# Optimization experiments

Measured on AMD Instinct MI355X. Metric: run time of the kernel, lower is better.

## Reference

```python
import jax, jax.numpy as jnp
import numpy as np

jax.config.update("jax_enable_x64", True)

PRIME = (1 << 31) - 1  # Mersenne prime; products with <2^31 operands fit in int64
N_DIGITS = 16
N_ARY = 32
EMB = 64
NUM_EMB = 100000    # importance-weight table rows
NUM_BUCKETS = 65536  # shared bucket table rows
NUM_HASHES = 2

_rng = np.random.RandomState(42)
SEQ_A = jnp.asarray(_rng.randint(1, PRIME, size=(N_DIGITS,)), dtype=jnp.int64)   # per-position keys for prefix hash
HASH_A = jnp.asarray(_rng.randint(1, PRIME, size=(NUM_HASHES,)), dtype=jnp.int64)
HASH_B = jnp.asarray(_rng.randint(0, PRIME, size=(NUM_HASHES,)), dtype=jnp.int64)


def _prefix_hashes(seq):
    # seq: [B, D] int64 sense codes, 0 = padding (mask_zero: zeros contribute nothing)
    h = jnp.cumsum(SEQ_A[None, :] * (seq.astype(jnp.int64) % PRIME), axis=-1) % PRIME  # [B, D]
    # pad_trailing_zeroes=True: positions past the code length repeat the last valid hash
    lengths = jnp.sum(seq != 0, axis=-1, keepdims=True)               # [B, 1]
    pos = jnp.arange(seq.shape[-1], dtype=jnp.int64)[None, :]
    idx = jnp.minimum(pos, jnp.maximum(lengths - 1, 0))
    return jnp.take_along_axis(h, idx, axis=-1)                        # [B, D]


def setup_inputs() -> dict:
    key = jax.random.key(0)
    k1, k2, k3, k4 = jax.random.split(key, 4)
    B = 4096
    input_sequence = jax.random.randint(k1, (B, N_DIGITS), 0, N_ARY, dtype=jnp.int64)
    t_representation = jax.random.normal(k2, (B, N_DIGITS, EMB), dtype=jnp.float32)
    importance_weights = jax.random.normal(k3, (NUM_EMB, NUM_HASHES), dtype=jnp.float32)
    bucket_table = jax.random.normal(k4, (NUM_BUCKETS, N_ARY * EMB), dtype=jnp.float32) * 0.02
    return {
        "input_sequence": input_sequence,
        "t_representation": t_representation,
        "importance_weights": importance_weights,
        "bucket_table": bucket_table,
    }


def reference(input_sequence, t_representation, importance_weights, bucket_table):
    ids = _prefix_hashes(input_sequence)                  # [B, D] prefix hash ids
    w = importance_weights[ids % NUM_EMB]                 # [B, D, H] importance weights
    emb = jnp.zeros(ids.shape + (bucket_table.shape[-1],), dtype=bucket_table.dtype)
    for h in range(NUM_HASHES):
        bucket = ((HASH_A[h] * ids + HASH_B[h]) % PRIME) % NUM_BUCKETS
        emb = emb + w[..., h:h + 1] * bucket_table[bucket]  # [B, D, N_ARY*EMB]
    B, D = ids.shape
    t_weight = emb.reshape(B, D, N_ARY, EMB).astype(t_representation.dtype)
    # torch.matmul(t_weight, rep.unsqueeze(-1)).squeeze(-1) -> [B, D, N_ARY]
    return jnp.einsum('bdae,bde->bda', t_weight, t_representation)
```

## Files before the change

### kernel.cpp

```cpp
#include <hip/hip_runtime.h>
#include <stdint.h>

#define PRIME 2147483647LL
#define NUM_EMB 100000
#define NUM_BUCKETS 65536
#define EMB 64
#define N_ARY 32
#define NDIG 16

struct HashConsts {
  long long seqA[NDIG];
  long long hashA[2];
  long long hashB[2];
};

__global__ __launch_bounds__(256) void hash_logits_kernel(
    const int* __restrict__ seq,
    const float* __restrict__ rep,
    const float* __restrict__ iw,
    const float* __restrict__ bt,
    float* __restrict__ out,
    HashConsts hc)
{
  const int bid  = blockIdx.x;
  const int b    = bid >> 2;
  const int wave = threadIdx.x >> 6;
  const int d    = ((bid & 3) << 2) | wave;
  const int lane = threadIdx.x & 63;
  const int g    = lane >> 4;
  const int sub  = lane & 15;

  const int* srow = seq + b * NDIG;
  int v[NDIG];
  int len = 0;
#pragma unroll
  for (int j = 0; j < NDIG; ++j) { v[j] = srow[j]; len += (v[j] != 0); }
  int idx = min(d, max(len - 1, 0));
  long long acc = 0;
#pragma unroll
  for (int j = 0; j < NDIG; ++j) {
    if (j <= idx) acc += hc.seqA[j] * (long long)v[j];
  }
  const long long id = acc % PRIME;

  const int widx = (int)(id % NUM_EMB);
  const float w0 = iw[widx * 2 + 0];
  const float w1 = iw[widx * 2 + 1];
  const unsigned int bk0 =
      (unsigned int)((hc.hashA[0] * id + hc.hashB[0]) % PRIME) & (NUM_BUCKETS - 1);
  const unsigned int bk1 =
      (unsigned int)((hc.hashA[1] * id + hc.hashB[1]) % PRIME) & (NUM_BUCKETS - 1);

  const float4* row0 = (const float4*)(bt + (size_t)bk0 * (N_ARY * EMB));
  const float4* row1 = (const float4*)(bt + (size_t)bk1 * (N_ARY * EMB));
  const float4 r = *(const float4*)(rep + ((size_t)b * NDIG + d) * EMB + sub * 4);

  float s[8];
#pragma unroll
  for (int k = 0; k < 8; ++k) {
    float4 v0 = row0[lane + 64 * k];
    float4 v1 = row1[lane + 64 * k];
    float ex = w0 * v0.x + w1 * v1.x;
    float ey = w0 * v0.y + w1 * v1.y;
    float ez = w0 * v0.z + w1 * v1.z;
    float ew = w0 * v0.w + w1 * v1.w;
    s[k] = ex * r.x + ey * r.y + ez * r.z + ew * r.w;
  }
#pragma unroll
  for (int m = 1; m <= 8; m <<= 1) {
#pragma unroll
    for (int k = 0; k < 8; ++k) s[k] += __shfl_xor(s[k], m, 64);
  }
  if (sub == 0) {
    float* obase = out + ((size_t)b * NDIG + d) * N_ARY + g;
#pragma unroll
    for (int k = 0; k < 8; ++k) obase[4 * k] = s[k];
  }
}

extern "C" void kernel_launch(void* const* d_in, const int* in_sizes, int n_in,
                              void* d_out, int out_size, void* d_ws, size_t ws_size,
                              hipStream_t stream) {
  uint32_t mt[624];
  int mti;
  mt[0] = 42u;
  for (int i = 1; i < 624; ++i)
    mt[i] = 1812433253u * (mt[i - 1] ^ (mt[i - 1] >> 30)) + (uint32_t)i;
  mti = 624;
  auto next32 = [&]() -> uint32_t {
    if (mti >= 624) {
      for (int i = 0; i < 624; ++i) {
        uint32_t y = (mt[i] & 0x80000000u) | (mt[(i + 1) % 624] & 0x7fffffffu);
        uint32_t x = mt[(i + 397) % 624] ^ (y >> 1);
        if (y & 1u) x ^= 2567483615u;
        mt[i] = x;
      }
      mti = 0;
    }
    uint32_t y = mt[mti++];
    y ^= y >> 11;
    y ^= (y << 7) & 2636928640u;
    y ^= (y << 15) & 4022730752u;
    y ^= y >> 18;
    return y;
  };
  auto draw = [&](uint32_t rng_incl) -> uint32_t {
    uint32_t val;
    do { val = next32() & 0x7FFFFFFFu; } while (val > rng_incl);
    return val;
  };
  HashConsts hc;
  for (int i = 0; i < NDIG; ++i) hc.seqA[i] = 1LL + (long long)draw(2147483645u);
  for (int i = 0; i < 2; ++i)    hc.hashA[i] = 1LL + (long long)draw(2147483645u);
  for (int i = 0; i < 2; ++i)    hc.hashB[i] = (long long)draw(2147483646u);

  const int*   seq = (const int*)d_in[0];
  const float* rep = (const float*)d_in[1];
  const float* iw  = (const float*)d_in[2];
  const float* bt  = (const float*)d_in[3];
  float*       out = (float*)d_out;

  const int B = in_sizes[0] / NDIG;
  dim3 grid(B * 4), block(256);
  hipLaunchKernelGGL(hash_logits_kernel, grid, block, 0, stream,
                     seq, rep, iw, bt, out, hc);
}
```

Baseline: 720.4 us.

## Process four digit positions per wave with Mersenne reduction and scalarized bucket addresses

Each block now handles a whole batch row, with every wave computing four digit positions instead of one. The 64-bit modulo is replaced by Mersenne-prime folding, and the ids, weights and bucket bases are made wave-uniform with readfirstlane. Eight independent row gathers are issued per iteration to raise memory-level parallelism. In exchange the grid shrinks fourfold and register pressure rises, and launch_bounds now requests 4 blocks per SM.

```diff
diff --git a/kernel.cpp b/kernel.cpp
--- a/kernel.cpp
+++ b/kernel.cpp
@@ -14,7 +14,7 @@
   long long hashB[2];
 };
 
-__global__ __launch_bounds__(256) void hash_logits_kernel(
+__global__ __launch_bounds__(256, 4) void hash_logits_kernel(
     const int* __restrict__ seq,
     const float* __restrict__ rep,
     const float* __restrict__ iw,
@@ -22,59 +22,103 @@
     float* __restrict__ out,
     HashConsts hc)
 {
-  const int bid  = blockIdx.x;
-  const int b    = bid >> 2;
+  const int b    = blockIdx.x;
   const int wave = threadIdx.x >> 6;
-  const int d    = ((bid & 3) << 2) | wave;
   const int lane = threadIdx.x & 63;
   const int g    = lane >> 4;
   const int sub  = lane & 15;
+
+  float4 r[4];
+#pragma unroll
+  for (int i = 0; i < 4; ++i) {
+    const int d = 4 * wave + i;
+    r[i] = *(const float4*)(rep + ((size_t)b * NDIG + d) * EMB + sub * 4);
+  }
 
   const int* srow = seq + b * NDIG;
   int v[NDIG];
   int len = 0;
 #pragma unroll
   for (int j = 0; j < NDIG; ++j) { v[j] = srow[j]; len += (v[j] != 0); }
-  int idx = min(d, max(len - 1, 0));
+  const int lm1 = max(len - 1, 0);
+
+  int idxv[4];
+#pragma unroll
+  for (int i = 0; i < 4; ++i) idxv[i] = min(4 * wave + i, lm1);
+
+  long long cap[4];
   long long acc = 0;
 #pragma unroll
   for (int j = 0; j < NDIG; ++j) {
-    if (j <= idx) acc += hc.seqA[j] * (long long)v[j];
+    acc += hc.seqA[j] * (long long)v[j];
+#pragma unroll
+    for (int i = 0; i < 4; ++i)
+      if (j == idxv[i]) cap[i] = acc;
   }
-  const long long id = acc % PRIME;
 
-  const int widx = (int)(id % NUM_EMB);
-  const float w0 = iw[widx * 2 + 0];
-  const float w1 = iw[widx * 2 + 1];
-  const unsigned int bk0 =
-      (unsigned int)((hc.hashA[0] * id + hc.hashB[0]) % PRIME) & (NUM_BUCKETS - 1);
-  const unsigned int bk1 =
-      (unsigned int)((hc.hashA[1] * id + hc.hashB[1]) % PRIME) & (NUM_BUCKETS - 1);
+  const float4* base0[4];
+  const float4* base1[4];
+  float w0f[4], w1f[4];
+#pragma unroll
+  for (int i = 0; i < 4; ++i) {
+    unsigned long long x = (unsigned long long)cap[i];
+    x = (x & (unsigned long long)PRIME) + (x >> 31);
+    x = (x & (unsigned long long)PRIME) + (x >> 31);
+    unsigned int id = (unsigned int)x;
+    if (id >= (unsigned int)PRIME) id -= (unsigned int)PRIME;
+    id = (unsigned int)__builtin_amdgcn_readfirstlane((int)id);
 
-  const float4* row0 = (const float4*)(bt + (size_t)bk0 * (N_ARY * EMB));
-  const float4* row1 = (const float4*)(bt + (size_t)bk1 * (N_ARY * EMB));
-  const float4 r = *(const float4*)(rep + ((size_t)b * NDIG + d) * EMB + sub * 4);
+    const unsigned int widx = id % 100000u;
+    const float2 wv = *(const float2*)(iw + (size_t)widx * 2);
+    w0f[i] = __int_as_float(__builtin_amdgcn_readfirstlane(__float_as_int(wv.x)));
+    w1f[i] = __int_as_float(__builtin_amdgcn_readfirstlane(__float_as_int(wv.y)));
 
-  float s[8];
+#pragma unroll
+    for (int h = 0; h < 2; ++h) {
+      unsigned long long t =
+          (unsigned long long)hc.hashA[h] * id + (unsigned long long)hc.hashB[h];
+      t = (t & (unsigned long long)PRIME) + (t >> 31);
+      t = (t & (unsigned long long)PRIME) + (t >> 31);
+      unsigned int z = (unsigned int)t;
+      if (z >= (unsigned int)PRIME) z -= (unsigned int)PRIME;
+      const int bk = __builtin_amdgcn_readfirstlane((int)(z & (NUM_BUCKETS - 1)));
+      const float4* base = (const float4*)bt + ((size_t)(unsigned)bk << 9);
+      if (h == 0) base0[i] = base; else base1[i] = base;
+    }
+  }
+
+  float s[4][8];
 #pragma unroll
   for (int k = 0; k < 8; ++k) {
-    float4 v0 = row0[lane + 64 * k];
-    float4 v1 = row1[lane + 64 * k];
-    float ex = w0 * v0.x + w1 * v1.x;
-    float ey = w0 * v0.y + w1 * v1.y;
-    float ez = w0 * v0.z + w1 * v1.z;
-    float ew = w0 * v0.w + w1 * v1.w;
-    s[k] = ex * r.x + ey * r.y + ez * r.z + ew * r.w;
+    float4 a0[4], a1[4];
+#pragma unroll
+    for (int i = 0; i < 4; ++i) {
+      a0[i] = base0[i][lane + 64 * k];
+      a1[i] = base1[i][lane + 64 * k];
+    }
+#pragma unroll
+    for (int i = 0; i < 4; ++i) {
+      const float d0 = a0[i].x * r[i].x + a0[i].y * r[i].y + a0[i].z * r[i].z + a0[i].w * r[i].w;
+      const float d1 = a1[i].x * r[i].x + a1[i].y * r[i].y + a1[i].z * r[i].z + a1[i].w * r[i].w;
+      s[i][k] = w0f[i] * d0 + w1f[i] * d1;
+    }
   }
+
 #pragma unroll
-  for (int m = 1; m <= 8; m <<= 1) {
+  for (int m = 1; m <= 8; m <<= 1)
 #pragma unroll
-    for (int k = 0; k < 8; ++k) s[k] += __shfl_xor(s[k], m, 64);
-  }
+    for (int i = 0; i < 4; ++i)
+#pragma unroll
+      for (int k = 0; k < 8; ++k)
+        s[i][k] += __shfl_xor(s[i][k], m, 64);
+
   if (sub == 0) {
-    float* obase = out + ((size_t)b * NDIG + d) * N_ARY + g;
 #pragma unroll
-    for (int k = 0; k < 8; ++k) obase[4 * k] = s[k];
+    for (int i = 0; i < 4; ++i) {
+      float* obase = out + ((size_t)b * NDIG + (4 * wave + i)) * N_ARY + g;
+#pragma unroll
+      for (int k = 0; k < 8; ++k) obase[4 * k] = s[i][k];
+    }
   }
 }
 
@@ -121,7 +165,7 @@
   float*       out = (float*)d_out;
 
   const int B = in_sizes[0] / NDIG;
-  dim3 grid(B * 4), block(256);
+  dim3 grid(B), block(256);
   hipLaunchKernelGGL(hash_logits_kernel, grid, block, 0, stream,
                      seq, rep, iw, bt, out, hc);
 }
```

Result: no change. 726.9 us (+0.9%).
